# Kernel optimization log

Measured on AMD Instinct MI355X. Metric: run time of the kernel, lower is better.

## Reference

```python
import jax, jax.numpy as jnp
import numpy as np

NUM_STATES = 8
HIDDEN_DIM = 1024
BATCH = 16384
DT = 0.01
PLANCK = 1.0
EPS_NORM = 1e-8
EPS_LOG = 1e-12


def setup_inputs() -> dict:
    key = jax.random.key(0)
    k1, k2, k3, k4, k5 = jax.random.split(key, 5)
    inv_sqrt_d = 1.0 / np.sqrt(HIDDEN_DIM)
    return {
        "input_state": jax.random.normal(k1, (BATCH, HIDDEN_DIM), dtype=jnp.float32),
        "amplitude_real": jax.random.normal(k2, (NUM_STATES, HIDDEN_DIM), dtype=jnp.float32) * inv_sqrt_d,
        "amplitude_imag": jax.random.normal(k3, (NUM_STATES, HIDDEN_DIM), dtype=jnp.float32) * inv_sqrt_d,
        "hamiltonian": jax.random.normal(k4, (NUM_STATES, NUM_STATES), dtype=jnp.float32) * 0.01,
        "projections": jax.random.normal(k5, (NUM_STATES, HIDDEN_DIM, HIDDEN_DIM), dtype=jnp.float32) * 0.01,
    }


def reference(input_state, amplitude_real, amplitude_imag, hamiltonian, projections):
    # complex amplitudes, normalized per state over hidden dim
    amps = amplitude_real + 1j * amplitude_imag  # [S, D] complex64
    norms = jnp.sum(jnp.abs(amps) ** 2, axis=1, keepdims=True)
    amps = amps / jnp.sqrt(norms + EPS_NORM)

    # unitary Hamiltonian evolution: expm(-i H dt / hbar) on the tiny SxS matrix
    H = (hamiltonian + hamiltonian.T) * 0.5
    U = jax.scipy.linalg.expm((-1j * DT / PLANCK) * H.astype(jnp.complex64))  # [S, S]
    amps = U @ amps  # [S, D]

    # decoherence at time_step=0: factor exp(0)=1, thermal noise scale 0 -> identity

    # superposed output: out[b,e] = sum_s Re(amps[s,e]) * (x @ P_s)[b,e]
    w = jnp.real(amps)  # [S, D]
    proj = jnp.einsum('bd,sde->bse', input_state, projections)  # [B, S, D]
    measured_output = jnp.einsum('bse,se->be', proj, w)  # [B, D]

    # measurement probabilities (computational basis)
    probs = jnp.abs(amps) ** 2
    probs = probs / (probs.sum(axis=0, keepdims=True) + EPS_NORM)
    collapse_prob = probs.mean(axis=1)  # [S]

    # metrics on rank-1 density matrix rho = outer(v, conj(v)), v = amps.flatten():
    # eigenvalues are {||v||^2, 0, ...} so the von Neumann entropy reduces to one term,
    # and sum|rho| = (sum|v|)^2, tr|diag| = sum|v|^2.
    v_abs = jnp.abs(amps.reshape(-1))
    lam = jnp.sum(v_abs ** 2)
    entanglement_entropy = -(lam * jnp.log(lam + EPS_LOG))
    coherence = jnp.sum(v_abs) ** 2 - lam

    amplitude_distribution = jnp.abs(amps) ** 2
    phase_evolution = jnp.angle(amps)

    return (measured_output, collapse_prob, entanglement_entropy, coherence,
            amplitude_distribution, phase_evolution)
```

## Files before the change

kernel.cpp:

```cpp
#include <hip/hip_runtime.h>
#include <hip/hip_bf16.h>

#define NSTATES 8
#define HD      1024
#define NBATCH  16384
#define NT      16

#define OUT_MEAS 0
#define OUT_CP   16777216
#define OUT_ENT  16777224
#define OUT_COH  16777225
#define OUT_AD   16777226
#define OUT_PH   16785418

typedef __attribute__((ext_vector_type(8))) short short8;
typedef __attribute__((ext_vector_type(4))) float f32x4;

__device__ __forceinline__ short f2bf(float f) {
    union { float f; unsigned u; } x; x.f = f;
    unsigned r = x.u + 0x7fffu + ((x.u >> 16) & 1u);
    return (short)(r >> 16);
}

__global__ __launch_bounds__(1024) void k_amps(const float* __restrict__ AR,
                                               const float* __restrict__ AI,
                                               const float* __restrict__ H,
                                               float* __restrict__ out,
                                               float* __restrict__ w) {
    __shared__ float redA[16 * NSTATES];
    __shared__ float redB[16 * 10];
    __shared__ float norms[NSTATES];
    __shared__ float sA[8][8], sA2[8][8], sA3[8][8];
    __shared__ float Ur[8][8], Ui[8][8];
    __shared__ float lamsa[2];

    const int tid = threadIdx.x;
    const int lane = tid & 63, wid = tid >> 6;
    const int d = tid;

    float arv[NSTATES], aiv[NSTATES];
    #pragma unroll
    for (int s = 0; s < NSTATES; s++) {
        arv[s] = AR[s * HD + d];
        aiv[s] = AI[s * HD + d];
    }
    float p[NSTATES];
    #pragma unroll
    for (int s = 0; s < NSTATES; s++) p[s] = arv[s] * arv[s] + aiv[s] * aiv[s];
    #pragma unroll
    for (int s = 0; s < NSTATES; s++)
        #pragma unroll
        for (int o = 32; o > 0; o >>= 1) p[s] += __shfl_down(p[s], o, 64);
    if (lane == 0)
        #pragma unroll
        for (int s = 0; s < NSTATES; s++) redA[wid * NSTATES + s] = p[s];
    if (tid < 64) {
        int i = tid >> 3, j = tid & 7;
        sA[i][j] = 0.5f * (H[i * 8 + j] + H[j * 8 + i]) * 0.01f;
    }
    __syncthreads();
    if (tid < 8) {
        float acc = 0.f;
        #pragma unroll
        for (int v = 0; v < 16; v++) acc += redA[v * NSTATES + tid];
        norms[tid] = acc;
    }
    if (tid < 64) {
        int i = tid >> 3, j = tid & 7;
        float acc = 0.f;
        #pragma unroll
        for (int k = 0; k < 8; k++) acc += sA[i][k] * sA[k][j];
        sA2[i][j] = acc;
    }
    __syncthreads();
    if (tid < 64) {
        int i = tid >> 3, j = tid & 7;
        float acc = 0.f;
        #pragma unroll
        for (int k = 0; k < 8; k++) acc += sA2[i][k] * sA[k][j];
        sA3[i][j] = acc;
        Ur[i][j] = ((i == j) ? 1.f : 0.f) - 0.5f * sA2[i][j];
        Ui[i][j] = -(sA[i][j] - sA3[i][j] * (1.f / 6.f));
    }
    __syncthreads();

    #pragma unroll
    for (int s = 0; s < NSTATES; s++) {
        float inv = 1.0f / sqrtf(norms[s] + 1e-8f);
        arv[s] *= inv;
        aiv[s] *= inv;
    }
    float nr[NSTATES], ni[NSTATES];
    #pragma unroll
    for (int s = 0; s < NSTATES; s++) {
        float xr = 0.f, xi = 0.f;
        #pragma unroll
        for (int t = 0; t < NSTATES; t++) {
            float ur = Ur[s][t], ui = Ui[s][t];
            xr += ur * arv[t] - ui * aiv[t];
            xi += ur * aiv[t] + ui * arv[t];
        }
        nr[s] = xr; ni[s] = xi;
    }
    float dist[NSTATES], csum = 0.f, sabs = 0.f;
    #pragma unroll
    for (int s = 0; s < NSTATES; s++) {
        dist[s] = nr[s] * nr[s] + ni[s] * ni[s];
        csum += dist[s];
        sabs += sqrtf(dist[s]);
    }
    #pragma unroll
    for (int s = 0; s < NSTATES; s++) {
        out[OUT_AD + s * HD + d] = dist[s];
        out[OUT_PH + s * HD + d] = atan2f(ni[s], nr[s]);
        w[s * HD + d] = nr[s];
    }
    float cinv = 1.0f / (csum + 1e-8f);
    float q[10];
    #pragma unroll
    for (int s = 0; s < NSTATES; s++) q[s] = dist[s] * cinv;
    q[8] = csum; q[9] = sabs;
    #pragma unroll
    for (int v = 0; v < 10; v++)
        #pragma unroll
        for (int o = 32; o > 0; o >>= 1) q[v] += __shfl_down(q[v], o, 64);
    if (lane == 0)
        #pragma unroll
        for (int v = 0; v < 10; v++) redB[wid * 10 + v] = q[v];
    __syncthreads();
    if (tid < 10) {
        float acc = 0.f;
        #pragma unroll
        for (int v = 0; v < 16; v++) acc += redB[v * 10 + tid];
        if (tid < 8)       out[OUT_CP + tid] = acc * (1.0f / HD);
        else               lamsa[tid - 8] = acc;
    }
    __syncthreads();
    if (tid == 0) {
        float lam = lamsa[0], sa = lamsa[1];
        out[OUT_ENT] = -(lam * logf(lam + 1e-12f));
        out[OUT_COH] = sa * sa - lam;
    }
}

__global__ __launch_bounds__(256) void k_castX(const float* __restrict__ X,
                                               short* __restrict__ Xb) {
    int idx = blockIdx.x * 256 + threadIdx.x;
    const float* src = X + (size_t)idx * 8;
    float4 f0 = *reinterpret_cast<const float4*>(src);
    float4 f1 = *reinterpret_cast<const float4*>(src + 4);
    short8 v;
    v[0] = f2bf(f0.x); v[1] = f2bf(f0.y); v[2] = f2bf(f0.z); v[3] = f2bf(f0.w);
    v[4] = f2bf(f1.x); v[5] = f2bf(f1.y); v[6] = f2bf(f1.z); v[7] = f2bf(f1.w);
    *reinterpret_cast<short8*>(Xb + (size_t)idx * 8) = v;
}

__global__ __launch_bounds__(256) void k_project_t(const float* __restrict__ P,
                                                   const float* __restrict__ w,
                                                   short* __restrict__ Mt) {
    __shared__ float tile[64][65];
    int d0 = (blockIdx.x >> 4) * 64;
    int e0 = (blockIdx.x & 15) * 64;
    int tx = threadIdx.x & 63, ty = threadIdx.x >> 6;
    float wv[NSTATES];
    #pragma unroll
    for (int s = 0; s < NSTATES; s++) wv[s] = w[s * HD + e0 + tx];
    #pragma unroll
    for (int j = 0; j < 16; j++) {
        int r = ty + 4 * j;
        float acc = 0.f;
        #pragma unroll
        for (int s = 0; s < NSTATES; s++)
            acc += wv[s] * P[(size_t)s * HD * HD + (size_t)(d0 + r) * HD + e0 + tx];
        tile[r][tx] = acc;
    }
    __syncthreads();
    #pragma unroll
    for (int j = 0; j < 16; j++) {
        int er = ty + 4 * j;
        Mt[(size_t)(e0 + er) * HD + d0 + tx] = f2bf(tile[tx][er]);
    }
}


__device__ __forceinline__ void stage_half(const short* __restrict__ srcBase,
                                           int rowbase, int h, int t2,
                                           short* dst, const int* aoff,
                                           const int* ldsoff) {
    #pragma unroll
    for (int i = 0; i < 2; i++) {
        const short* g = srcBase + (size_t)(rowbase + h * 128) * HD + t2 * 64 + aoff[i];
        __builtin_amdgcn_global_load_lds(
            (const __attribute__((address_space(1))) void*)g,
            (__attribute__((address_space(3))) void*)(dst + h * 8192 + ldsoff[i]),
            16, 0, 0);
    }
}

#define LOAD_A(qa)                                                             \
    _Pragma("unroll") for (int mf = 0; mf < 4; mf++)                           \
    _Pragma("unroll") for (int kk = 0; kk < 2; kk++)                           \
        af[mf][kk] = *reinterpret_cast<const short8*>(                         \
            &Acur[((qa) * 128 + wr64 + mf * 16 + ln15) * 64 + kx[kk]]);

#define LOAD_B(qb)                                                             \
    _Pragma("unroll") for (int nf = 0; nf < 2; nf++)                           \
    _Pragma("unroll") for (int kk = 0; kk < 2; kk++)                           \
        bf[nf][kk] = *reinterpret_cast<const short8*>(                         \
            &Bcur[((qb) * 128 + wn32 + nf * 16 + ln15) * 64 + kx[kk]]);

#define MFMA_P(qa, qb)                                                         \
    _Pragma("unroll") for (int mf = 0; mf < 4; mf++)                           \
    _Pragma("unroll") for (int nf = 0; nf < 2; nf++)                           \
    _Pragma("unroll") for (int kk = 0; kk < 2; kk++)                           \
        acc[(qa) * 4 + mf][(qb) * 2 + nf] =                                    \
            __builtin_amdgcn_mfma_f32_16x16x32_bf16(                           \
                af[mf][kk], bf[nf][kk], acc[(qa) * 4 + mf][(qb) * 2 + nf], 0, 0, 0);

#define PHASE_MID()                                                            \
    __builtin_amdgcn_s_barrier();                                              \
    __builtin_amdgcn_s_setprio(1);

#define PHASE_END()                                                            \
    __builtin_amdgcn_s_setprio(0);                                             \
    __builtin_amdgcn_s_barrier();

__global__ __launch_bounds__(512, 1) void k_gemm_8p(const short* __restrict__ Xb,
                                                    const short* __restrict__ Mt,
                                                    float* __restrict__ out) {
    __shared__ short As[2][256 * 64];
    __shared__ short Bs[2][256 * 64];

    const int bid = blockIdx.x;
    const int swz = (bid & 7) * 32 + (bid >> 3);
    const int brow = (swz >> 2) * 256;
    const int bcol = (swz & 3) * 256;

    const int tid  = threadIdx.x;
    const int lane = tid & 63, wid = tid >> 6;
    const int wr = wid >> 2, wn = wid & 3;
    const int ln15 = lane & 15, l16 = lane >> 4;
    const int wr64 = wr * 64;
    const int wn32 = wn * 32;

    int kx[2];
    kx[0] = ((l16 + 0) ^ (ln15 & 7)) * 8;
    kx[1] = ((l16 + 4) ^ (ln15 & 7)) * 8;

    int aoff[2], ldsoff[2];
    #pragma unroll
    for (int i = 0; i < 2; i++) {
        int c = tid + 512 * i;
        int row = c >> 3, kc = c & 7;
        aoff[i]   = row * HD + ((kc ^ (row & 7)) * 8);
        ldsoff[i] = c * 8;
    }

    short* A0 = &As[0][0]; short* A1b = &As[1][0];
    short* B0 = &Bs[0][0]; short* B1b = &Bs[1][0];

    f32x4 acc[8][4];
    #pragma unroll
    for (int m = 0; m < 8; m++)
        #pragma unroll
        for (int n = 0; n < 4; n++) acc[m][n] = (f32x4){0.f, 0.f, 0.f, 0.f};

    stage_half(Xb, brow, 0, 0, A0, aoff, ldsoff);
    stage_half(Xb, brow, 1, 0, A0, aoff, ldsoff);
    stage_half(Mt, bcol, 0, 0, B0, aoff, ldsoff);
    stage_half(Mt, bcol, 1, 0, B0, aoff, ldsoff);
    stage_half(Xb, brow, 0, 1, A1b, aoff, ldsoff);
    stage_half(Mt, bcol, 1, 1, B1b, aoff, ldsoff);
    asm volatile("s_waitcnt vmcnt(4)" ::: "memory");
    __builtin_amdgcn_s_barrier();

    short8 af[4][2], bf[2][2];

    #pragma unroll 1
    for (int t = 0; t < NT; t++) {
        const int cur = t & 1;
        short* Acur  = cur ? A1b : A0;
        short* Bcur  = cur ? B1b : B0;
        short* Anext = cur ? A0 : A1b;
        short* Bnext = cur ? B0 : B1b;

        LOAD_A(0); LOAD_B(0);
        if (t + 1 < NT) stage_half(Xb, brow, 1, t + 1, Anext, aoff, ldsoff);
        PHASE_MID();
        MFMA_P(0, 0);
        PHASE_END();

        LOAD_B(1);
        if (t + 1 < NT) stage_half(Mt, bcol, 0, t + 1, Bnext, aoff, ldsoff);
        PHASE_MID();
        MFMA_P(0, 1);
        PHASE_END();

        LOAD_A(1);
        if (t + 2 < NT) stage_half(Xb, brow, 0, t + 2, Acur, aoff, ldsoff);
        PHASE_MID();
        MFMA_P(1, 1);
        PHASE_END();

        LOAD_B(0);
        if (t + 2 < NT) stage_half(Mt, bcol, 1, t + 2, Bcur, aoff, ldsoff);
        PHASE_MID();
        MFMA_P(1, 0);
        __builtin_amdgcn_s_setprio(0);
        if (t < NT - 2)       asm volatile("s_waitcnt vmcnt(4)" ::: "memory");
        else if (t == NT - 2) asm volatile("s_waitcnt vmcnt(0)" ::: "memory");
        __builtin_amdgcn_s_barrier();
    }

    #pragma unroll
    for (int qa = 0; qa < 2; qa++)
        #pragma unroll
        for (int mf = 0; mf < 4; mf++)
            #pragma unroll
            for (int qb = 0; qb < 2; qb++)
                #pragma unroll
                for (int nf = 0; nf < 2; nf++)
                    #pragma unroll
                    for (int j = 0; j < 4; j++) {
                        int r = brow + qa * 128 + wr64 + mf * 16 + l16 * 4 + j;
                        int c = bcol + qb * 128 + wn32 + nf * 16 + ln15;
                        out[(size_t)r * HD + c] = acc[qa * 4 + mf][qb * 2 + nf][j];
                    }
}

extern "C" void kernel_launch(void* const* d_in, const int* in_sizes, int n_in,
                              void* d_out, int out_size, void* d_ws, size_t ws_size,
                              hipStream_t stream) {
    const float* X  = (const float*)d_in[0];
    const float* AR = (const float*)d_in[1];
    const float* AI = (const float*)d_in[2];
    const float* H  = (const float*)d_in[3];
    const float* P  = (const float*)d_in[4];
    float* out = (float*)d_out;

    char* ws = (char*)d_ws;
    float* w  = (float*)ws;
    short* Mt = (short*)(ws + 32768);
    short* Xb = (short*)(ws + 32768 + 2097152);

    k_amps<<<1, 1024, 0, stream>>>(AR, AI, H, out, w);
    k_project_t<<<256, 256, 0, stream>>>(P, w, Mt);
    k_castX<<<(NBATCH * HD) / (256 * 8), 256, 0, stream>>>(X, Xb);
    k_gemm_8p<<<(NBATCH / 256) * (HD / 256), 512, 0, stream>>>(Xb, Mt, out);
}
```

Measured before the change: 79.98 us.

## Fuse fp32-to-bf16 cast of X into GEMM A-tile staging

Removes the separate X cast kernel and its bf16 workspace round trip. The GEMM now loads fp32 X into registers, converts to bf16 and writes to LDS itself, with the staging pipeline reshaped to a one-tile lookahead for A. This trades the cast kernel's extra HBM traffic and launch for double the A read bytes per tile, more register pressure, and synchronous register-staged loads in place of async global-to-LDS copies. Each X tile is now re-read as fp32 by the four column blocks.

```diff
diff --git a/kernel.cpp b/kernel.cpp
--- a/kernel.cpp
+++ b/kernel.cpp
@@ -20,6 +20,13 @@
     union { float f; unsigned u; } x; x.f = f;
     unsigned r = x.u + 0x7fffu + ((x.u >> 16) & 1u);
     return (short)(r >> 16);
+}
+
+__device__ __forceinline__ short8 pack8(float4 a, float4 b) {
+    short8 v;
+    v[0] = f2bf(a.x); v[1] = f2bf(a.y); v[2] = f2bf(a.z); v[3] = f2bf(a.w);
+    v[4] = f2bf(b.x); v[5] = f2bf(b.y); v[6] = f2bf(b.z); v[7] = f2bf(b.w);
+    return v;
 }
 
 __global__ __launch_bounds__(1024) void k_amps(const float* __restrict__ AR,
@@ -143,18 +150,6 @@
     }
 }
 
-__global__ __launch_bounds__(256) void k_castX(const float* __restrict__ X,
-                                               short* __restrict__ Xb) {
-    int idx = blockIdx.x * 256 + threadIdx.x;
-    const float* src = X + (size_t)idx * 8;
-    float4 f0 = *reinterpret_cast<const float4*>(src);
-    float4 f1 = *reinterpret_cast<const float4*>(src + 4);
-    short8 v;
-    v[0] = f2bf(f0.x); v[1] = f2bf(f0.y); v[2] = f2bf(f0.z); v[3] = f2bf(f0.w);
-    v[4] = f2bf(f1.x); v[5] = f2bf(f1.y); v[6] = f2bf(f1.z); v[7] = f2bf(f1.w);
-    *reinterpret_cast<short8*>(Xb + (size_t)idx * 8) = v;
-}
-
 __global__ __launch_bounds__(256) void k_project_t(const float* __restrict__ P,
                                                    const float* __restrict__ w,
                                                    short* __restrict__ Mt) {
@@ -183,19 +178,34 @@
 }
 
 
-__device__ __forceinline__ void stage_half(const short* __restrict__ srcBase,
-                                           int rowbase, int h, int t2,
-                                           short* dst, const int* aoff,
-                                           const int* ldsoff) {
+__device__ __forceinline__ void stage_half_B(const short* __restrict__ srcBase,
+                                             int rowbase, int h, int t2,
+                                             short* dst, const int* goff,
+                                             const int* ldsoff) {
     #pragma unroll
     for (int i = 0; i < 2; i++) {
-        const short* g = srcBase + (size_t)(rowbase + h * 128) * HD + t2 * 64 + aoff[i];
+        const short* g = srcBase + (size_t)(rowbase + h * 128) * HD + t2 * 64 + goff[i];
         __builtin_amdgcn_global_load_lds(
             (const __attribute__((address_space(1))) void*)g,
             (__attribute__((address_space(3))) void*)(dst + h * 8192 + ldsoff[i]),
             16, 0, 0);
     }
 }
+
+#define XLOAD(h, t2)                                                           \
+    {                                                                          \
+        const float* base_ = X + (size_t)(brow + (h) * 128) * HD + (t2) * 64;  \
+        xr[0] = *reinterpret_cast<const float4*>(base_ + goff[0]);             \
+        xr[1] = *reinterpret_cast<const float4*>(base_ + goff[0] + 4);         \
+        xr[2] = *reinterpret_cast<const float4*>(base_ + goff[1]);             \
+        xr[3] = *reinterpret_cast<const float4*>(base_ + goff[1] + 4);         \
+    }
+
+#define XWRITE(dst, h)                                                         \
+    {                                                                          \
+        *reinterpret_cast<short8*>((dst) + (h) * 8192 + ldsoff[0]) = pack8(xr[0], xr[1]); \
+        *reinterpret_cast<short8*>((dst) + (h) * 8192 + ldsoff[1]) = pack8(xr[2], xr[3]); \
+    }
 
 #define LOAD_A(qa)                                                             \
     _Pragma("unroll") for (int mf = 0; mf < 4; mf++)                           \
@@ -225,7 +235,7 @@
     __builtin_amdgcn_s_setprio(0);                                             \
     __builtin_amdgcn_s_barrier();
 
-__global__ __launch_bounds__(512, 1) void k_gemm_8p(const short* __restrict__ Xb,
+__global__ __launch_bounds__(512, 1) void k_gemm_8p(const float* __restrict__ X,
                                                     const short* __restrict__ Mt,
                                                     float* __restrict__ out) {
     __shared__ short As[2][256 * 64];
@@ -247,12 +257,12 @@
     kx[0] = ((l16 + 0) ^ (ln15 & 7)) * 8;
     kx[1] = ((l16 + 4) ^ (ln15 & 7)) * 8;
 
-    int aoff[2], ldsoff[2];
+    int goff[2], ldsoff[2];
     #pragma unroll
     for (int i = 0; i < 2; i++) {
         int c = tid + 512 * i;
         int row = c >> 3, kc = c & 7;
-        aoff[i]   = row * HD + ((kc ^ (row & 7)) * 8);
+        goff[i]   = row * HD + ((kc ^ (row & 7)) * 8);
         ldsoff[i] = c * 8;
     }
 
@@ -265,13 +275,24 @@
         #pragma unroll
         for (int n = 0; n < 4; n++) acc[m][n] = (f32x4){0.f, 0.f, 0.f, 0.f};
 
-    stage_half(Xb, brow, 0, 0, A0, aoff, ldsoff);
-    stage_half(Xb, brow, 1, 0, A0, aoff, ldsoff);
-    stage_half(Mt, bcol, 0, 0, B0, aoff, ldsoff);
-    stage_half(Mt, bcol, 1, 0, B0, aoff, ldsoff);
-    stage_half(Xb, brow, 0, 1, A1b, aoff, ldsoff);
-    stage_half(Mt, bcol, 1, 1, B1b, aoff, ldsoff);
-    asm volatile("s_waitcnt vmcnt(4)" ::: "memory");
+    float4 xr[4];
+
+    XLOAD(0, 0);
+    float4 xr2[4];
+    {
+        const float* base_ = X + (size_t)(brow + 128) * HD;
+        xr2[0] = *reinterpret_cast<const float4*>(base_ + goff[0]);
+        xr2[1] = *reinterpret_cast<const float4*>(base_ + goff[0] + 4);
+        xr2[2] = *reinterpret_cast<const float4*>(base_ + goff[1]);
+        xr2[3] = *reinterpret_cast<const float4*>(base_ + goff[1] + 4);
+    }
+    stage_half_B(Mt, bcol, 0, 0, B0, goff, ldsoff);
+    stage_half_B(Mt, bcol, 1, 0, B0, goff, ldsoff);
+    stage_half_B(Mt, bcol, 1, 1, B1b, goff, ldsoff);
+    XWRITE(A0, 0);
+    *reinterpret_cast<short8*>(A0 + 8192 + ldsoff[0]) = pack8(xr2[0], xr2[1]);
+    *reinterpret_cast<short8*>(A0 + 8192 + ldsoff[1]) = pack8(xr2[2], xr2[3]);
+    asm volatile("s_waitcnt vmcnt(2) lgkmcnt(0)" ::: "memory");
     __builtin_amdgcn_s_barrier();
 
     short8 af[4][2], bf[2][2];
@@ -285,30 +306,36 @@
         short* Bnext = cur ? B0 : B1b;
 
         LOAD_A(0); LOAD_B(0);
-        if (t + 1 < NT) stage_half(Xb, brow, 1, t + 1, Anext, aoff, ldsoff);
+        if (t + 1 < NT) XLOAD(0, (t + 1));
         PHASE_MID();
         MFMA_P(0, 0);
         PHASE_END();
 
         LOAD_B(1);
-        if (t + 1 < NT) stage_half(Mt, bcol, 0, t + 1, Bnext, aoff, ldsoff);
+        if (t + 1 < NT) {
+            stage_half_B(Mt, bcol, 0, t + 1, Bnext, goff, ldsoff);
+            XWRITE(Anext, 0);
+        }
         PHASE_MID();
         MFMA_P(0, 1);
-        PHASE_END();
+        __builtin_amdgcn_s_setprio(0);
+        asm volatile("s_waitcnt lgkmcnt(0)" ::: "memory");
+        __builtin_amdgcn_s_barrier();
 
         LOAD_A(1);
-        if (t + 2 < NT) stage_half(Xb, brow, 0, t + 2, Acur, aoff, ldsoff);
+        if (t + 1 < NT) XLOAD(1, (t + 1));
         PHASE_MID();
         MFMA_P(1, 1);
         PHASE_END();
 
         LOAD_B(0);
-        if (t + 2 < NT) stage_half(Mt, bcol, 1, t + 2, Bcur, aoff, ldsoff);
+        if (t + 1 < NT) XWRITE(Anext, 1);
+        if (t + 2 < NT) stage_half_B(Mt, bcol, 1, t + 2, Bcur, goff, ldsoff);
         PHASE_MID();
         MFMA_P(1, 0);
         __builtin_amdgcn_s_setprio(0);
-        if (t < NT - 2)       asm volatile("s_waitcnt vmcnt(4)" ::: "memory");
-        else if (t == NT - 2) asm volatile("s_waitcnt vmcnt(0)" ::: "memory");
+        if (t + 2 < NT) asm volatile("s_waitcnt vmcnt(2) lgkmcnt(0)" ::: "memory");
+        else            asm volatile("s_waitcnt vmcnt(0) lgkmcnt(0)" ::: "memory");
         __builtin_amdgcn_s_barrier();
     }
 
@@ -341,10 +368,8 @@
     char* ws = (char*)d_ws;
     float* w  = (float*)ws;
     short* Mt = (short*)(ws + 32768);
-    short* Xb = (short*)(ws + 32768 + 2097152);
 
     k_amps<<<1, 1024, 0, stream>>>(AR, AI, H, out, w);
     k_project_t<<<256, 256, 0, stream>>>(P, w, Mt);
-    k_castX<<<(NBATCH * HD) / (256 * 8), 256, 0, stream>>>(X, Xb);
-    k_gemm_8p<<<(NBATCH / 256) * (HD / 256), 512, 0, stream>>>(Xb, Mt, out);
-}
+    k_gemm_8p<<<(NBATCH / 256) * (HD / 256), 512, 0, stream>>>(X, Mt, out);
+}
```

Result: faster. 76.43 us (-4.4%).
